# Performance work log

Hardware: AMD Instinct MI355X
Metric: run time of the kernel (lower is better)

## Reference

```python
import jax, jax.numpy as jnp
import numpy as np

B, T, I, H, O = 128, 64, 512, 1024, 512
EPS = 0.01
N_MAX = 12  # static max ACT ponder steps per timestep (halts at ~2 steps at init)


def setup_inputs() -> dict:
    key = jax.random.key(0)
    ks = jax.random.split(key, 10)
    k = 1.0 / np.sqrt(H)
    u = lambda kk, shape: jax.random.uniform(kk, shape, jnp.float32, -k, k)
    return {
        "x": jax.random.normal(ks[0], (B, T, I), jnp.float32),
        "s0": jax.random.normal(ks[1], (1, B, H), jnp.float32) * 0.1,
        "w_ih": u(ks[2], (H, 1 + I)),
        "w_hh": u(ks[3], (H, H)),
        "b_ih": u(ks[4], (H,)),
        "b_hh": u(ks[5], (H,)),
        "w_halt": u(ks[6], (1, H)),
        "b_halt": u(ks[7], (1,)),
        "w_out": u(ks[8], (O, H)),
        "b_out": u(ks[9], (O,)),
    }


def _binarize_st(p):
    # Binarize autograd.Function: forward -> 1 where p > 0 (sigmoid outputs are
    # always positive, zeroed halted entries stay 0); backward -> identity (STE).
    return p + jax.lax.stop_gradient(jnp.where(p > 0, 1.0, 0.0) - p)


def reference(x, s0, w_ih, w_hh, b_ih, b_hh, w_halt, b_halt, w_out, b_out):
    def cell(inp, h):  # inp [B,1+I], h [B,H] -> tanh RNN cell
        return jnp.tanh(inp @ w_ih.T + b_ih + h @ w_hh.T + b_hh)

    def timestep(h_carry, x_t):  # h_carry [B,H], x_t [B,I]
        ones = jnp.ones((B, 1), x_t.dtype)
        x1 = jnp.concatenate([ones, x_t], axis=1)          # flag=1: first ponder step
        x0 = jnp.concatenate([ones * 0.0, x_t], axis=1)    # flag=0: continued pondering
        # ponder step 0 (always contributes for every sample)
        h = cell(x1, h_carry)
        out = h @ w_out.T + b_out                 # [B,O]
        p = jax.nn.sigmoid(h @ w_halt.T + b_halt) # [B,1]
        w = _binarize_st(p)
        out_acc = out * w
        h_acc = h * w
        cum = p[:, 0]
        # ponder value is only assigned when a sample halts at step 0 (original bug kept)
        pond = jnp.where(cum >= 1.0 - EPS, 2.0, 0.0)

        def ponder_step(carry, _):
            h_prev, cum, out_acc, h_acc = carry
            active = (cum < 1.0 - EPS).astype(h_prev.dtype)[:, None]  # [B,1]
            h = cell(x0, h_prev) * active
            out = (h @ w_out.T + b_out) * active
            p = jax.nn.sigmoid(h @ w_halt.T + b_halt) * active
            w = _binarize_st(p)
            return (h, cum + p[:, 0], out_acc + out * w, h_acc + h * w), None

        (h, cum, out_acc, h_acc), _ = jax.lax.scan(
            ponder_step, (h, cum, out_acc, h_acc), None, length=N_MAX - 1)
        # next-timestep hidden is the binarized-weight accumulation of states
        return h_acc, (out_acc, pond)

    h_last, (outputs, ponder) = jax.lax.scan(timestep, s0[0], jnp.swapaxes(x, 0, 1))
    return jnp.swapaxes(outputs, 0, 1), jnp.swapaxes(ponder, 0, 1)  # [B,T,O], [B,T]
```

## Files before the change

### kernel.cpp

```cpp
#include <hip/hip_runtime.h>
#include <hip/hip_cooperative_groups.h>
#include <math.h>

namespace cg = cooperative_groups;

#define NB 128
#define NT 64
#define NI 512
#define NH 1024
#define NO 512
#define PONDOFF (NB*NT*NO)

extern __shared__ float smem[];

__device__ __forceinline__ void group_barrier(unsigned* ctr, unsigned target, int tid)
{
    __syncthreads();
    if (tid == 0) {
        __hip_atomic_fetch_add(ctr, 1u, __ATOMIC_RELEASE, __HIP_MEMORY_SCOPE_AGENT);
        while (__hip_atomic_load(ctr, __ATOMIC_RELAXED, __HIP_MEMORY_SCOPE_AGENT) < target)
            __builtin_amdgcn_s_sleep(1);
    }
    if (tid < 64)
        __builtin_amdgcn_fence(__ATOMIC_ACQUIRE, "agent");
    __syncthreads();
}

__global__ void __launch_bounds__(1024, 1)
arnn_coop(const float* __restrict__ x, const float* __restrict__ s0,
          const float* __restrict__ w_ih, const float* __restrict__ w_hh,
          const float* __restrict__ b_ih, const float* __restrict__ b_hh,
          const float* __restrict__ w_halt, const float* __restrict__ b_halt,
          const float* __restrict__ w_out, const float* __restrict__ b_out,
          float* __restrict__ out, float* __restrict__ ws)
{
    cg::grid_group grid = cg::this_grid();
    const int tid = threadIdx.x;
    const int bid = blockIdx.x;
    const int gid = bid * 1024 + tid;

    float* wihT  = ws;
    float* hbuf  = wihT + NI*NH;
    float* habuf = hbuf + NB*2*NH;
    unsigned* ctrA = (unsigned*)(habuf + 2*NB*NH);

    const int gp = bid >> 5, lb = bid & 31;

    __shared__ float s_whalt[NH + (NH/16)*4];
    __shared__ int   s_t[16];
    __shared__ float s_cum[16];
    __shared__ int   s_n[16];
    __shared__ int   s_et[16], s_en[16];
    __shared__ unsigned char s_sl[16];
    __shared__ unsigned char s_run[16];
    __shared__ unsigned char s_mode[16];
    __shared__ unsigned char s_epi[16];

    for (int e = gid; e < NI*NH; e += 256*1024) {
        const int i = e >> 10, jj = e & 1023;
        wihT[e] = w_ih[jj*(NI+1) + 1 + i];
    }
    if (gid < 8*32)
        __hip_atomic_store(&ctrA[gid], 0u, __ATOMIC_RELAXED, __HIP_MEMORY_SCOPE_AGENT);
    for (int e = tid; e < 1024*32; e += 1024) {
        const int k = e & 1023, jj = e >> 10;
        const float v = w_hh[(lb*32 + jj)*NH + k];
        const int su = (jj >> 1) ^ ((k >> 6) & 15);
        smem[k*32 + su*2 + (jj & 1)] = v;
    }
    {
        const int j = tid;
        s_whalt[j + ((j >> 4) << 2)] = w_halt[j];
    }
    if (tid < 16) {
        s_t[tid] = 0; s_cum[tid] = 0.0f; s_n[tid] = 0;
        s_et[tid] = 0; s_en[tid] = 0;
        s_sl[tid] = 0; s_run[tid] = 1; s_mode[tid] = 0; s_epi[tid] = 0;
    }
    grid.sync();

    unsigned* ctr = ctrA + gp*32;

    const int w    = tid >> 6;
    const int lane = tid & 63;
    const int rq   = w >> 2;
    const int co   = w & 3;
    const int up   = lane & 3;
    const int ks   = lane >> 2;
    const int u    = co*4 + up;
    const int jg   = lb*32 + u*2;
    const int b0   = gp*16 + rq*4;
    const bool k0  = (ks == 0);
    const int ldsb = ks*2048 + ((u ^ ks) << 1);

    const float bh  = b_halt[0];
    const float bias0 = k0 ? (b_ih[jg]   + b_hh[jg])   : 0.0f;
    const float bias1 = k0 ? (b_ih[jg+1] + b_hh[jg+1]) : 0.0f;
    const float w0a   = k0 ? w_ih[jg*(NI+1)]     : 0.0f;
    const float w0b   = k0 ? w_ih[(jg+1)*(NI+1)] : 0.0f;

    const int   eo = lb*16 + (lane & 15);
    const int   eq = lane >> 4;
    const int   eb = gp*16 + w;
    const float bo = b_out[eo];

    auto decide_p = [&](int slot) -> float {
        const float* hr = hbuf + ((gp*16 + w)*2 + slot)*NH + lane*16;
        float d = 0.0f;
        #pragma unroll
        for (int q = 0; q < 16; q += 4) {
            const float4 hv = *(const float4*)(hr + q);
            const float4 wv = *(const float4*)(&s_whalt[lane*20 + q]);
            d += hv.x*wv.x + hv.y*wv.y + hv.z*wv.z + hv.w*wv.w;
        }
        d += __shfl_xor(d, 1);  d += __shfl_xor(d, 2);  d += __shfl_xor(d, 4);
        d += __shfl_xor(d, 8);  d += __shfl_xor(d, 16); d += __shfl_xor(d, 32);
        return 1.0f / (1.0f + expf(-(d + bh)));
    };

    float xw[4][2];
    float hacc[4][2];

    unsigned gen = 0;
    for (;;) {
        if (s_epi[w]) {
            const int et = s_et[w];
            const float* ha = habuf + (et&1)*(NB*NH) + eb*NH + eq*256;
            const float* wq = w_out + eo*NH + eq*256;
            float acc = 0.0f;
            #pragma unroll 4
            for (int jj2 = 0; jj2 < 256; jj2 += 4) {
                const float4 hv = *(const float4*)(ha + jj2);
                const float4 wv = *(const float4*)(wq + jj2);
                acc += hv.x*wv.x + hv.y*wv.y + hv.z*wv.z + hv.w*wv.w;
            }
            acc += __shfl_xor(acc, 16); acc += __shfl_xor(acc, 32);
            if (eq == 0) out[(eb*NT + et)*NO + eo] = acc + (float)s_en[w]*bo;
        }
        int ex[4], md[4], tt[4], sl[4];
        #pragma unroll
        for (int r = 0; r < 4; ++r) {
            const int rr = rq*4 + r;
            ex[r] = s_run[rr]; md[r] = s_mode[rr]; tt[r] = s_t[rr]; sl[r] = s_sl[rr];
        }
        if (ex[0] | ex[1] | ex[2] | ex[3]) {
            #pragma unroll
            for (int r = 0; r < 4; ++r) {
                if (ex[r] && md[r] == 0) {
                    float o0 = bias0, o1 = bias1;
                    const float* xr = x + ((b0+r)*NT + tt[r])*NI + ks*32;
                    const float* wp = wihT + (ks*32)*NH + jg;
                    #pragma unroll 4
                    for (int i = 0; i < 32; i += 4) {
                        const float4 xv = *(const float4*)(xr + i);
                        const float2 wa = *(const float2*)(wp + (i  )*NH);
                        const float2 wb = *(const float2*)(wp + (i+1)*NH);
                        const float2 wc = *(const float2*)(wp + (i+2)*NH);
                        const float2 wd = *(const float2*)(wp + (i+3)*NH);
                        o0 += xv.x*wa.x + xv.y*wb.x + xv.z*wc.x + xv.w*wd.x;
                        o1 += xv.x*wa.y + xv.y*wb.y + xv.z*wc.y + xv.w*wd.y;
                    }
                    xw[r][0] = o0; xw[r][1] = o1;
                }
            }
            float a[4][2];
            const float* hp[4];
            #pragma unroll
            for (int r = 0; r < 4; ++r) {
                const int b = b0 + r;
                a[r][0] = xw[r][0] + (md[r] == 0 ? w0a : 0.0f);
                a[r][1] = xw[r][1] + (md[r] == 0 ? w0b : 0.0f);
                if (!ex[r])           hp[r] = hbuf + (b*2)*NH + ks*64;
                else if (md[r] == 0)  hp[r] = (tt[r] == 0 ? s0 + b*NH
                                              : habuf + ((tt[r]-1)&1)*(NB*NH) + b*NH) + ks*64;
                else                  hp[r] = hbuf + (b*2 + sl[r])*NH + ks*64;
            }
            #pragma unroll 4
            for (int kc = 0; kc < 64; kc += 4) {
                const float4 h0 = *(const float4*)(hp[0] + kc);
                const float4 h1 = *(const float4*)(hp[1] + kc);
                const float4 h2 = *(const float4*)(hp[2] + kc);
                const float4 h3 = *(const float4*)(hp[3] + kc);
                const float2 wa = *(const float2*)(smem + ldsb + (kc  )*32);
                const float2 wb = *(const float2*)(smem + ldsb + (kc+1)*32);
                const float2 wc = *(const float2*)(smem + ldsb + (kc+2)*32);
                const float2 wd = *(const float2*)(smem + ldsb + (kc+3)*32);
                a[0][0] += h0.x*wa.x + h0.y*wb.x + h0.z*wc.x + h0.w*wd.x;
                a[0][1] += h0.x*wa.y + h0.y*wb.y + h0.z*wc.y + h0.w*wd.y;
                a[1][0] += h1.x*wa.x + h1.y*wb.x + h1.z*wc.x + h1.w*wd.x;
                a[1][1] += h1.x*wa.y + h1.y*wb.y + h1.z*wc.y + h1.w*wd.y;
                a[2][0] += h2.x*wa.x + h2.y*wb.x + h2.z*wc.x + h2.w*wd.x;
                a[2][1] += h2.x*wa.y + h2.y*wb.y + h2.z*wc.y + h2.w*wd.y;
                a[3][0] += h3.x*wa.x + h3.y*wb.x + h3.z*wc.x + h3.w*wd.x;
                a[3][1] += h3.x*wa.y + h3.y*wb.y + h3.z*wc.y + h3.w*wd.y;
            }
            #pragma unroll
            for (int r = 0; r < 4; ++r)
                #pragma unroll
                for (int c = 0; c < 2; ++c) {
                    float v = a[r][c];
                    v += __shfl_xor(v, 4);  v += __shfl_xor(v, 8);
                    v += __shfl_xor(v, 16); v += __shfl_xor(v, 32);
                    a[r][c] = v;
                }
            if (k0) {
                #pragma unroll
                for (int r = 0; r < 4; ++r) {
                    if (ex[r]) {
                        const float ha = tanhf(a[r][0]), hb = tanhf(a[r][1]);
                        const int b = b0 + r;
                        *(float2*)(hbuf + (b*2 + (sl[r]^1))*NH + jg) = make_float2(ha, hb);
                        if (md[r] == 0) { hacc[r][0] = ha;  hacc[r][1] = hb; }
                        else            { hacc[r][0] += ha; hacc[r][1] += hb; }
                        *(float2*)(habuf + (tt[r]&1)*(NB*NH) + b*NH + jg) =
                            make_float2(hacc[r][0], hacc[r][1]);
                    }
                }
            }
        }
        ++gen; group_barrier(ctr, 32*gen, tid);
        const int exw = s_run[w];
        float p = 0.0f;
        if (exw) p = decide_p(s_sl[w] ^ 1);
        if (lane == 0) {
            int newepi = 0;
            if (exw) {
                const int t = s_t[w];
                float cum; int n;
                if (s_mode[w] == 0) {
                    cum = p; n = 1;
                    if (lb == 0) out[PONDOFF + (gp*16 + w)*NT + t] = (p >= 0.99f) ? 2.0f : 0.0f;
                } else {
                    cum = s_cum[w] + p; n = s_n[w] + 1;
                }
                s_cum[w] = cum; s_n[w] = n;
                s_sl[w] ^= 1;
                if ((cum < 0.99f) && n < 12) {
                    s_mode[w] = 1;
                } else {
                    newepi = 1; s_et[w] = t; s_en[w] = n;
                    if (t == NT-1) s_run[w] = 0;
                    else { s_t[w] = t + 1; s_mode[w] = 0; }
                }
            }
            s_epi[w] = newepi;
        }
        __syncthreads();
        const int al = (lane < 16) ? (s_run[lane] | s_epi[lane]) : 0;
        if (__ballot(al) == 0ULL) break;
    }
}

extern "C" void kernel_launch(void* const* d_in, const int* in_sizes, int n_in,
                              void* d_out, int out_size, void* d_ws, size_t ws_size,
                              hipStream_t stream) {
    const float* x      = (const float*)d_in[0];
    const float* s0     = (const float*)d_in[1];
    const float* w_ih   = (const float*)d_in[2];
    const float* w_hh   = (const float*)d_in[3];
    const float* b_ih   = (const float*)d_in[4];
    const float* b_hh   = (const float*)d_in[5];
    const float* w_halt = (const float*)d_in[6];
    const float* b_halt = (const float*)d_in[7];
    const float* w_out  = (const float*)d_in[8];
    const float* b_out  = (const float*)d_in[9];
    float* out = (float*)d_out;
    float* ws  = (float*)d_ws;

    static const int kLds = 131072;
    hipFuncSetAttribute((const void*)arnn_coop,
                        hipFuncAttributeMaxDynamicSharedMemorySize, kLds);

    void* args[] = { (void*)&x, (void*)&s0, (void*)&w_ih, (void*)&w_hh,
                     (void*)&b_ih, (void*)&b_hh, (void*)&w_halt, (void*)&b_halt,
                     (void*)&w_out, (void*)&b_out, (void*)&out, (void*)&ws };
    hipLaunchCooperativeKernel((void*)arnn_coop, dim3(256), dim3(1024), args, kLds, stream);
}
```

Before: 9.415 ms.

## Replace barrier fences with coherent sc0/sc1 loads/stores and software-pipelined prefetch

Shared hidden-state buffers are now read and written with inline-asm global loads/stores carrying sc0 sc1 cache-coherence bits. This lets the grid barrier drop its release ordering and the acquire fence that invalidated caches. The h-vector inner loop and the output epilogue get a manual 3-deep prefetch pipeline with explicit vmcnt waits, overlapping global-load latency with FMAs. Correctness now depends on hand-written waitcnt counts and the coherence bits, and the bypassed caches may raise latency per load.

```diff
diff --git a/kernel.cpp b/kernel.cpp
--- a/kernel.cpp
+++ b/kernel.cpp
@@ -13,16 +13,38 @@
 
 extern __shared__ float smem[];
 
+__device__ __forceinline__ float4 ld4cc(const float* p) {
+    float4 v;
+    asm volatile("global_load_dwordx4 %0, %1, off sc0 sc1" : "=v"(v) : "v"(p));
+    return v;
+}
+__device__ __forceinline__ float4 ld4nc(const float* p) {
+    float4 v;
+    asm volatile("global_load_dwordx4 %0, %1, off" : "=v"(v) : "v"(p));
+    return v;
+}
+__device__ __forceinline__ void st2cc(float* p, float a, float b) {
+    float2 v = make_float2(a, b);
+    asm volatile("global_store_dwordx2 %0, %1, off sc0 sc1"
+                 :: "v"(p), "v"(v) : "memory");
+}
+#define WAITV(N) do {                                            \
+    asm volatile("s_waitcnt vmcnt(" #N ")" ::: "memory");        \
+    __builtin_amdgcn_sched_barrier(0);                           \
+} while (0)
+__device__ __forceinline__ void vdrain() {
+    asm volatile("s_waitcnt vmcnt(0)" ::: "memory");
+}
+
 __device__ __forceinline__ void group_barrier(unsigned* ctr, unsigned target, int tid)
 {
+    vdrain();
     __syncthreads();
     if (tid == 0) {
-        __hip_atomic_fetch_add(ctr, 1u, __ATOMIC_RELEASE, __HIP_MEMORY_SCOPE_AGENT);
+        __hip_atomic_fetch_add(ctr, 1u, __ATOMIC_RELAXED, __HIP_MEMORY_SCOPE_AGENT);
         while (__hip_atomic_load(ctr, __ATOMIC_RELAXED, __HIP_MEMORY_SCOPE_AGENT) < target)
             __builtin_amdgcn_s_sleep(1);
     }
-    if (tid < 64)
-        __builtin_amdgcn_fence(__ATOMIC_ACQUIRE, "agent");
     __syncthreads();
 }
 
@@ -106,12 +128,27 @@
 
     auto decide_p = [&](int slot) -> float {
         const float* hr = hbuf + ((gp*16 + w)*2 + slot)*NH + lane*16;
+        float4 hv0 = ld4cc(hr);
+        float4 hv1 = ld4cc(hr + 4);
+        float4 hv2 = ld4cc(hr + 8);
+        float4 hv3 = ld4cc(hr + 12);
+        WAITV(0);
         float d = 0.0f;
-        #pragma unroll
-        for (int q = 0; q < 16; q += 4) {
-            const float4 hv = *(const float4*)(hr + q);
-            const float4 wv = *(const float4*)(&s_whalt[lane*20 + q]);
-            d += hv.x*wv.x + hv.y*wv.y + hv.z*wv.z + hv.w*wv.w;
+        {
+            const float4 wv = *(const float4*)(&s_whalt[lane*20 + 0]);
+            d += hv0.x*wv.x + hv0.y*wv.y + hv0.z*wv.z + hv0.w*wv.w;
+        }
+        {
+            const float4 wv = *(const float4*)(&s_whalt[lane*20 + 4]);
+            d += hv1.x*wv.x + hv1.y*wv.y + hv1.z*wv.z + hv1.w*wv.w;
+        }
+        {
+            const float4 wv = *(const float4*)(&s_whalt[lane*20 + 8]);
+            d += hv2.x*wv.x + hv2.y*wv.y + hv2.z*wv.z + hv2.w*wv.w;
+        }
+        {
+            const float4 wv = *(const float4*)(&s_whalt[lane*20 + 12]);
+            d += hv3.x*wv.x + hv3.y*wv.y + hv3.z*wv.z + hv3.w*wv.w;
         }
         d += __shfl_xor(d, 1);  d += __shfl_xor(d, 2);  d += __shfl_xor(d, 4);
         d += __shfl_xor(d, 8);  d += __shfl_xor(d, 16); d += __shfl_xor(d, 32);
@@ -125,14 +162,34 @@
     for (;;) {
         if (s_epi[w]) {
             const int et = s_et[w];
-            const float* ha = habuf + (et&1)*(NB*NH) + eb*NH + eq*256;
-            const float* wq = w_out + eo*NH + eq*256;
+            const float* hap = habuf + (et&1)*(NB*NH) + eb*NH + eq*256;
+            const float* wq  = w_out + eo*NH + eq*256;
             float acc = 0.0f;
-            #pragma unroll 4
-            for (int jj2 = 0; jj2 < 256; jj2 += 4) {
-                const float4 hv = *(const float4*)(ha + jj2);
-                const float4 wv = *(const float4*)(wq + jj2);
-                acc += hv.x*wv.x + hv.y*wv.y + hv.z*wv.z + hv.w*wv.w;
+            float4 eh[3][2], ew[3][2];
+            vdrain();
+            #pragma unroll
+            for (int G = 0; G < 3; ++G) {
+                eh[G][0] = ld4cc(hap + G*8);
+                eh[G][1] = ld4cc(hap + G*8 + 4);
+                ew[G][0] = ld4nc(wq + G*8);
+                ew[G][1] = ld4nc(wq + G*8 + 4);
+            }
+            #pragma unroll
+            for (int G = 0; G < 32; ++G) {
+                const int s = G % 3;
+                if (G <= 29)      WAITV(8);
+                else if (G == 30) WAITV(4);
+                else              WAITV(0);
+                acc += eh[s][0].x*ew[s][0].x + eh[s][0].y*ew[s][0].y
+                     + eh[s][0].z*ew[s][0].z + eh[s][0].w*ew[s][0].w;
+                acc += eh[s][1].x*ew[s][1].x + eh[s][1].y*ew[s][1].y
+                     + eh[s][1].z*ew[s][1].z + eh[s][1].w*ew[s][1].w;
+                if (G <= 28) {
+                    eh[s][0] = ld4cc(hap + (G+3)*8);
+                    eh[s][1] = ld4cc(hap + (G+3)*8 + 4);
+                    ew[s][0] = ld4nc(wq + (G+3)*8);
+                    ew[s][1] = ld4nc(wq + (G+3)*8 + 4);
+                }
             }
             acc += __shfl_xor(acc, 16); acc += __shfl_xor(acc, 32);
             if (eq == 0) out[(eb*NT + et)*NO + eo] = acc + (float)s_en[w]*bo;
@@ -175,12 +232,25 @@
                                               : habuf + ((tt[r]-1)&1)*(NB*NH) + b*NH) + ks*64;
                 else                  hp[r] = hbuf + (b*2 + sl[r])*NH + ks*64;
             }
-            #pragma unroll 4
-            for (int kc = 0; kc < 64; kc += 4) {
-                const float4 h0 = *(const float4*)(hp[0] + kc);
-                const float4 h1 = *(const float4*)(hp[1] + kc);
-                const float4 h2 = *(const float4*)(hp[2] + kc);
-                const float4 h3 = *(const float4*)(hp[3] + kc);
+            vdrain();
+            float4 hr3[3][4];
+            #pragma unroll
+            for (int g = 0; g < 3; ++g) {
+                #pragma unroll
+                for (int r = 0; r < 4; ++r)
+                    hr3[g][r] = ld4cc(hp[r] + g*4);
+            }
+            #pragma unroll
+            for (int g = 0; g < 16; ++g) {
+                const int s = g % 3;
+                if (g <= 13)      WAITV(8);
+                else if (g == 14) WAITV(4);
+                else              WAITV(0);
+                const float4 h0 = hr3[s][0];
+                const float4 h1 = hr3[s][1];
+                const float4 h2 = hr3[s][2];
+                const float4 h3 = hr3[s][3];
+                const int kc = g*4;
                 const float2 wa = *(const float2*)(smem + ldsb + (kc  )*32);
                 const float2 wb = *(const float2*)(smem + ldsb + (kc+1)*32);
                 const float2 wc = *(const float2*)(smem + ldsb + (kc+2)*32);
@@ -193,6 +263,11 @@
                 a[2][1] += h2.x*wa.y + h2.y*wb.y + h2.z*wc.y + h2.w*wd.y;
                 a[3][0] += h3.x*wa.x + h3.y*wb.x + h3.z*wc.x + h3.w*wd.x;
                 a[3][1] += h3.x*wa.y + h3.y*wb.y + h3.z*wc.y + h3.w*wd.y;
+                if (g <= 12) {
+                    #pragma unroll
+                    for (int r = 0; r < 4; ++r)
+                        hr3[s][r] = ld4cc(hp[r] + (g+3)*4);
+                }
             }
             #pragma unroll
             for (int r = 0; r < 4; ++r)
@@ -209,11 +284,11 @@
                     if (ex[r]) {
                         const float ha = tanhf(a[r][0]), hb = tanhf(a[r][1]);
                         const int b = b0 + r;
-                        *(float2*)(hbuf + (b*2 + (sl[r]^1))*NH + jg) = make_float2(ha, hb);
+                        st2cc(hbuf + (b*2 + (sl[r]^1))*NH + jg, ha, hb);
                         if (md[r] == 0) { hacc[r][0] = ha;  hacc[r][1] = hb; }
                         else            { hacc[r][0] += ha; hacc[r][1] += hb; }
-                        *(float2*)(habuf + (tt[r]&1)*(NB*NH) + b*NH + jg) =
-                            make_float2(hacc[r][0], hacc[r][1]);
+                        st2cc(habuf + (tt[r]&1)*(NB*NH) + b*NH + jg,
+                              hacc[r][0], hacc[r][1]);
                     }
                 }
             }
@@ -268,11 +343,12 @@
     float* ws  = (float*)d_ws;
 
     static const int kLds = 131072;
-    hipFuncSetAttribute((const void*)arnn_coop,
-                        hipFuncAttributeMaxDynamicSharedMemorySize, kLds);
+    (void)hipFuncSetAttribute((const void*)arnn_coop,
+                              hipFuncAttributeMaxDynamicSharedMemorySize, kLds);
 
     void* args[] = { (void*)&x, (void*)&s0, (void*)&w_ih, (void*)&w_hh,
                      (void*)&b_ih, (void*)&b_hh, (void*)&w_halt, (void*)&b_halt,
                      (void*)&w_out, (void*)&b_out, (void*)&out, (void*)&ws };
-    hipLaunchCooperativeKernel((void*)arnn_coop, dim3(256), dim3(1024), args, kLds, stream);
-}
+    (void)hipLaunchCooperativeKernel((void*)arnn_coop, dim3(256), dim3(1024),
+                                     args, kLds, stream);
+}
```

After: 11.78 ms. 1.25x slower.
